# Optimization experiments

Measured on AMD Instinct MI355X. Metric: run time of the kernel, lower is better.

Reference implementation:

```python
import jax, jax.numpy as jnp
import numpy as np
from jax import lax

D, H, HD, DEPTH = 200, 10, 20, 12   # embed_dim, heads, head_dim, depth
NCH, A = 64, 8                       # EEG channels x time windows -> 512 patches (+cls)
NUM_REL = (2 * NCH - 1) * (2 * A - 1) + 3  # 1908


def make_rel_index(wh, ww):
    # exact port of the torch relative_position_index construction
    coords = np.stack(np.meshgrid(np.arange(wh), np.arange(ww), indexing='ij')).reshape(2, -1)
    rel = (coords[:, :, None] - coords[:, None, :]).transpose(1, 2, 0)
    rel[..., 0] += wh - 1
    rel[..., 1] += ww - 1
    rel[..., 0] *= 2 * ww - 1
    n = wh * ww + 1
    num_rel = (2 * wh - 1) * (2 * ww - 1) + 3
    idx = np.zeros((n, n), dtype=np.int32)
    idx[1:, 1:] = rel.sum(-1)
    idx[0, :] = num_rel - 3
    idx[:, 0] = num_rel - 2
    idx[0, 0] = num_rel - 1
    return idx


def gelu(x):
    return jax.nn.gelu(x, approximate=False)


def layer_norm(x, g, b, eps=1e-6):
    m = x.mean(-1, keepdims=True)
    v = ((x - m) ** 2).mean(-1, keepdims=True)
    return (x - m) * lax.rsqrt(v + eps) * g + b


def group_norm(x, g, b, groups=4, eps=1e-5):
    B, C, Hh, W = x.shape
    xr = x.reshape(B, groups, C // groups, Hh, W)
    m = xr.mean((2, 3, 4), keepdims=True)
    v = ((xr - m) ** 2).mean((2, 3, 4), keepdims=True)
    xr = ((xr - m) * lax.rsqrt(v + eps)).reshape(B, C, Hh, W)
    return xr * g[None, :, None, None] + b[None, :, None, None]


def conv2d(x, w, b, stride, pad):
    y = lax.conv_general_dilated(x, w, window_strides=stride, padding=pad,
                                 dimension_numbers=('NCHW', 'OIHW', 'NCHW'))
    return y + b[None, :, None, None]


def setup_inputs() -> dict:
    B = 8
    key = jax.random.key(0)
    ks = iter(jax.random.split(key, 40))
    rn = lambda shape, s=0.02: jax.random.normal(next(ks), shape, dtype=jnp.float32) * s
    z = lambda shape: jnp.zeros(shape, jnp.float32)
    o = lambda shape: jnp.ones(shape, jnp.float32)
    inp = {}
    inp['x'] = jax.random.normal(next(ks), (B, NCH, A, 200), dtype=jnp.float32)
    inp['conv1_w'] = rn((8, 1, 1, 15), 0.1); inp['conv1_b'] = z(8)
    inp['gn1_g'] = o(8); inp['gn1_b'] = z(8)
    inp['conv2_w'] = rn((8, 8, 1, 3), 0.1); inp['conv2_b'] = z(8)
    inp['gn2_g'] = o(8); inp['gn2_b'] = z(8)
    inp['conv3_w'] = rn((8, 8, 1, 3), 0.1); inp['conv3_b'] = z(8)
    inp['gn3_g'] = o(8); inp['gn3_b'] = z(8)
    inp['cls_token'] = rn((1, 1, D)); inp['pos_embed'] = rn((1, NCH + 1, D))
    inp['time_embed'] = rn((1, 16, D))
    inp['ln1_g'] = o((DEPTH, D)); inp['ln1_b'] = z((DEPTH, D))
    inp['qkv_w'] = rn((DEPTH, 3 * D, D))
    inp['rel_bias_table'] = rn((DEPTH, NUM_REL, H))
    inp['proj_w'] = rn((DEPTH, D, D)); inp['proj_b'] = z((DEPTH, D))
    inp['gamma1'] = 0.1 * o((DEPTH, D))
    inp['ln2_g'] = o((DEPTH, D)); inp['ln2_b'] = z((DEPTH, D))
    inp['fc1_w'] = rn((DEPTH, 4 * D, D)); inp['fc1_b'] = z((DEPTH, 4 * D))
    inp['fc2_w'] = rn((DEPTH, D, 4 * D)); inp['fc2_b'] = z((DEPTH, D))
    inp['gamma2'] = 0.1 * o((DEPTH, D))
    inp['fc_norm_g'] = o(D); inp['fc_norm_b'] = z(D)
    inp['head_w'] = rn((4, D)); inp['head_b'] = z(4)
    inp['rel_pos_index'] = jnp.asarray(make_rel_index(NCH, A))
    return inp


def reference(x, conv1_w, conv1_b, gn1_g, gn1_b, conv2_w, conv2_b, gn2_g, gn2_b,
              conv3_w, conv3_b, gn3_g, gn3_b, cls_token, pos_embed, time_embed,
              ln1_g, ln1_b, qkv_w, rel_bias_table, proj_w, proj_b, gamma1,
              ln2_g, ln2_b, fc1_w, fc1_b, fc2_w, fc2_b, gamma2,
              fc_norm_g, fc_norm_b, head_w, head_b, rel_pos_index):
    B = x.shape[0]
    # TemporalConv patch embed: (B, NCH, A, 200) -> (B, NCH*A, D)
    h = x.reshape(B, 1, NCH * A, -1)
    h = gelu(group_norm(conv2d(h, conv1_w, conv1_b, (1, 8), [(0, 0), (7, 7)]), gn1_g, gn1_b))
    h = gelu(group_norm(conv2d(h, conv2_w, conv2_b, (1, 1), [(0, 0), (1, 1)]), gn2_g, gn2_b))
    h = gelu(group_norm(conv2d(h, conv3_w, conv3_b, (1, 1), [(0, 0), (1, 1)]), gn3_g, gn3_b))
    h = h.transpose(0, 2, 3, 1).reshape(B, NCH * A, D)  # 'B C NA T -> B NA (T C)'
    # cls token + per-electrode pos embed + temporal embed
    h = jnp.concatenate([jnp.broadcast_to(cls_token, (B, 1, D)), h], axis=1)
    pos_p = jnp.repeat(pos_embed[:, 1:, None, :], A, axis=2).reshape(1, NCH * A, D)
    h = h + jnp.concatenate([pos_embed[:, :1], pos_p], axis=1)
    te = jnp.broadcast_to(time_embed[:, None, :A, :], (1, NCH, A, D)).reshape(1, NCH * A, D)
    h = jnp.concatenate([h[:, :1], h[:, 1:] + te], axis=1)
    N = h.shape[1]  # 513
    scale = HD ** -0.5
    for d in range(DEPTH):
        y = layer_norm(h, ln1_g[d], ln1_b[d])
        qkv = (y @ qkv_w[d].T).reshape(B, N, 3, H, HD).transpose(2, 0, 3, 1, 4)
        q, k, v = qkv[0], qkv[1], qkv[2]
        attn = jnp.einsum('bhnd,bhmd->bhnm', q * scale, k)
        attn = attn + rel_bias_table[d][rel_pos_index].transpose(2, 0, 1)[None]
        attn = jax.nn.softmax(attn, axis=-1)
        o = jnp.einsum('bhnm,bhmd->bhnd', attn, v)
        o = o.transpose(0, 2, 1, 3).reshape(B, N, D) @ proj_w[d].T + proj_b[d]
        h = h + gamma1[d] * o
        y = layer_norm(h, ln2_g[d], ln2_b[d])
        y = gelu(y @ fc1_w[d].T + fc1_b[d]) @ fc2_w[d].T + fc2_b[d]
        h = h + gamma2[d] * y
    pooled = layer_norm(h[:, 1:].mean(1), fc_norm_g, fc_norm_b)  # use_mean_pooling
    return pooled @ head_w.T + head_b
```

## Files before the change

### kernel.cpp

```cpp
#include <hip/hip_runtime.h>
#include <math.h>

#define DEV static __device__ __forceinline__

typedef __attribute__((ext_vector_type(8))) short bf16x8;
typedef __attribute__((ext_vector_type(4))) float f32x4;

DEV float gelu_exact(float x) {
    return 0.5f * x * (1.0f + erff(x * 0.70710678118654752f));
}

DEV short f2bf(float f) {
    union { float f; unsigned u; } v; v.f = f;
    unsigned r = v.u + 0x7FFF + ((v.u >> 16) & 1);
    return (short)(r >> 16);
}

DEV float bf2f(unsigned short b) {
    union { unsigned u; float f; } v; v.u = ((unsigned)b) << 16;
    return v.f;
}

DEV unsigned pack2bf(float a, float b) {
    return ((unsigned)(unsigned short)f2bf(a)) | (((unsigned)(unsigned short)f2bf(b)) << 16);
}

DEV void gload_lds16(const void* g, void* lds) {
    __builtin_amdgcn_global_load_lds(
        (const __attribute__((address_space(1))) void*)g,
        (__attribute__((address_space(3))) void*)lds, 16, 0, 0);
}

__global__ void conv1_kernel(const float* __restrict__ x, const float* __restrict__ w,
                             const float* __restrict__ bias, float* __restrict__ out) {
    int idx = blockIdx.x * blockDim.x + threadIdx.x;
    const int total = 8 * 8 * 512 * 25;
    if (idx >= total) return;
    int ow = idx % 25;
    int p  = (idx / 25) % 512;
    int oc = (idx / (25 * 512)) % 8;
    int b  = idx / (25 * 512 * 8);
    const float* xp = x + b * 512 * 200 + p * 200;
    const float* wp = w + oc * 15;
    float acc = bias[oc];
    int t0 = ow * 8 - 7;
#pragma unroll
    for (int k = 0; k < 15; k++) {
        int t = t0 + k;
        if (t >= 0 && t < 200) acc += wp[k] * xp[t];
    }
    out[idx] = acc;
}

__global__ void conv3x1_kernel(const float* __restrict__ in, const float* __restrict__ w,
                               const float* __restrict__ bias, float* __restrict__ out) {
    int idx = blockIdx.x * blockDim.x + threadIdx.x;
    const int total = 8 * 8 * 512 * 25;
    if (idx >= total) return;
    int ow = idx % 25;
    int p  = (idx / 25) % 512;
    int oc = (idx / 12800) & 7;
    int b  = idx / 102400;
    float acc = bias[oc];
#pragma unroll
    for (int ic = 0; ic < 8; ic++) {
        const float* ip = in + b * 102400 + ic * 12800 + p * 25;
        const float* wp = w + oc * 24 + ic * 3;
        if (ow > 0)  acc += wp[0] * ip[ow - 1];
        acc += wp[1] * ip[ow];
        if (ow < 24) acc += wp[2] * ip[ow + 1];
    }
    out[idx] = acc;
}

__global__ void gn_stats_kernel(const float* __restrict__ buf, float* __restrict__ stats) {
    int b = blockIdx.x >> 2, g = blockIdx.x & 3;
    const float* base = buf + b * 102400 + g * 2 * 12800;
    float s = 0.f, s2 = 0.f;
    for (int l = threadIdx.x; l < 25600; l += 256) {
        float v = base[l];
        s += v; s2 += v * v;
    }
    __shared__ float ss[256], ss2[256];
    ss[threadIdx.x] = s; ss2[threadIdx.x] = s2;
    __syncthreads();
    for (int o = 128; o; o >>= 1) {
        if (threadIdx.x < o) { ss[threadIdx.x] += ss[threadIdx.x + o]; ss2[threadIdx.x] += ss2[threadIdx.x + o]; }
        __syncthreads();
    }
    if (threadIdx.x == 0) {
        float m = ss[0] / 25600.f;
        float v = ss2[0] / 25600.f - m * m;
        stats[blockIdx.x * 2] = m;
        stats[blockIdx.x * 2 + 1] = v;
    }
}

__global__ void gn_apply_kernel(float* __restrict__ buf, const float* __restrict__ stats,
                                const float* __restrict__ g, const float* __restrict__ bb) {
    int idx = blockIdx.x * blockDim.x + threadIdx.x;
    if (idx >= 8 * 102400) return;
    int c = (idx / 12800) & 7;
    int b = idx / 102400;
    int grp = c >> 1;
    float m = stats[(b * 4 + grp) * 2];
    float v = stats[(b * 4 + grp) * 2 + 1];
    float val = (buf[idx] - m) * rsqrtf(v + 1e-5f) * g[c] + bb[c];
    buf[idx] = gelu_exact(val);
}

__global__ void embed_kernel(const float* __restrict__ conv, const float* __restrict__ cls,
                             const float* __restrict__ pos, const float* __restrict__ te,
                             float* __restrict__ h) {
    int idx = blockIdx.x * blockDim.x + threadIdx.x;
    if (idx >= 8 * 513 * 200) return;
    int d = idx % 200;
    int n = (idx / 200) % 513;
    int b = idx / (200 * 513);
    float val;
    if (n == 0) {
        val = cls[d] + pos[d];
    } else {
        int p = n - 1;
        int t = d >> 3;
        int c = d & 7;
        val = conv[b * 102400 + c * 12800 + p * 25 + t];
        int ch = p >> 3, tw = p & 7;
        val += pos[(1 + ch) * 200 + d] + te[tw * 200 + d];
    }
    h[idx] = val;
}

__global__ void convpad_kernel(const float* __restrict__ src, short* __restrict__ dst,
                               int R, int K, int KP) {
    int idx = blockIdx.x * blockDim.x + threadIdx.x;
    if (idx >= R * KP) return;
    int r = idx / KP, c = idx % KP;
    dst[idx] = (c < K) ? f2bf(src[r * K + c]) : (short)0;
}

__global__ __launch_bounds__(256) void bias_lds_kernel(const float* __restrict__ table,
                                                       const int* __restrict__ ridx,
                                                       short* __restrict__ bias) {
    __shared__ float tl[1908];
    const int qt = blockIdx.x, hh = blockIdx.y, d = blockIdx.z;
    const float* tab = table + d * 19080;
    for (int i = threadIdx.x; i < 1908; i += 256) tl[i] = tab[i * 10 + hh];
    __syncthreads();
    const int q0 = qt * 64;
    const int nrows = min(64, 513 - q0);
    short* obase = bias + ((size_t)d * 10 + hh) * 513 * 576;
    for (int lin = threadIdx.x; lin < nrows * 144; lin += 256) {
        int r = lin / 144, j = lin % 144;
        int q = q0 + r;
        const int* rp = ridx + q * 513;
        int k0 = j * 4;
        float v[4];
#pragma unroll
        for (int e = 0; e < 4; e++) {
            int k = k0 + e;
            v[e] = (k < 513) ? tl[rp[k]] : 0.f;
        }
        uint2 pk;
        pk.x = pack2bf(v[0], v[1]);
        pk.y = pack2bf(v[2], v[3]);
        *(uint2*)&obase[(size_t)q * 576 + k0] = pk;
    }
}

__global__ __launch_bounds__(256) void ln_kernel(const float* __restrict__ in,
                                                 const float* __restrict__ g,
                                                 const float* __restrict__ b,
                                                 short* __restrict__ out) {
    int row = blockIdx.x * 4 + (threadIdx.x >> 6);
    int lane = threadIdx.x & 63;
    const float* x = in + (size_t)row * 200;
    float v[4];
    float s = 0.f;
#pragma unroll
    for (int i = 0; i < 4; i++) {
        int d = lane + i * 64;
        v[i] = (d < 200) ? x[d] : 0.f;
        s += v[i];
    }
#pragma unroll
    for (int o = 32; o; o >>= 1) s += __shfl_xor(s, o);
    float mean = s * (1.f / 200.f);
    float s2 = 0.f;
#pragma unroll
    for (int i = 0; i < 4; i++) {
        int d = lane + i * 64;
        float dv = (d < 200) ? (v[i] - mean) : 0.f;
        s2 += dv * dv;
    }
#pragma unroll
    for (int o = 32; o; o >>= 1) s2 += __shfl_xor(s2, o);
    float rstd = rsqrtf(s2 * (1.f / 200.f) + 1e-6f);
#pragma unroll
    for (int i = 0; i < 4; i++) {
        int d = lane + i * 64;
        float val = (d < 200) ? (v[i] - mean) * rstd * g[d] + b[d] : 0.f;
        out[(size_t)row * 256 + d] = f2bf(val);
    }
}

template <int EPI, int BM, int BN>
__global__ __launch_bounds__(256) void gemm_bf(const short* __restrict__ A,
                                               const short* __restrict__ W,
                                               float* __restrict__ Cf,
                                               short* __restrict__ Cb,
                                               const float* __restrict__ res,
                                               const float* __restrict__ bias,
                                               const float* __restrict__ gamma,
                                               int M, int N, int KP, int ldc, int NPout,
                                               short* __restrict__ Qb = nullptr,
                                               short* __restrict__ Kb = nullptr,
                                               short* __restrict__ Vt = nullptr) {
    constexpr int WM = BM / 2, WN = BN / 2;
    constexpr int AM = WM / 16, BNr = WN / 16;
    constexpr int LOADS = (BM + BN) / 32;
    __shared__ __align__(16) short Ss[2][(BM + BN) * 64];

    const int tid = threadIdx.x;
    const int w = tid >> 6, l = tid & 63;
    const int wm = (w >> 1) * WM, wn = (w & 1) * WN;
    const int bm = blockIdx.y * BM, bn = blockIdx.x * BN;

    f32x4 acc[AM][BNr] = {};

    auto stage = [&](int buf, int k0) {
#pragma unroll
        for (int it = 0; it < LOADS; it++) {
            int lin = it * 256 + tid;
            int row = lin >> 3, slot = lin & 7;
            int srcslot = slot ^ (row & 7);
            const short* g;
            if (it * 32 < BM) {
                g = A + (size_t)(bm + row) * KP + k0 + srcslot * 8;
            } else {
                g = W + (size_t)(bn + row - BM) * KP + k0 + srcslot * 8;
            }
            gload_lds16(g, (char*)Ss[buf] + lin * 16);
        }
    };

    const int nk = KP >> 6;
    stage(0, 0);
    int cur = 0;
    for (int kstep = 0; kstep < nk; kstep++) {
        if (kstep + 1 < nk) {
            stage(cur ^ 1, (kstep + 1) << 6);
            if constexpr (LOADS == 6) asm volatile("s_waitcnt vmcnt(6)" ::: "memory");
            else                      asm volatile("s_waitcnt vmcnt(4)" ::: "memory");
        } else {
            asm volatile("s_waitcnt vmcnt(0)" ::: "memory");
        }
        __builtin_amdgcn_s_barrier();

        const char* Sc = (const char*)Ss[cur];
#pragma unroll
        for (int kk = 0; kk < 2; kk++) {
            const int kbyte = kk * 64 + (l >> 4) * 16;
            bf16x8 af[AM], bfr[BNr];
#pragma unroll
            for (int i = 0; i < AM; i++) {
                int r = wm + i * 16 + (l & 15);
                af[i] = *(const bf16x8*)(Sc + r * 128 + (kbyte ^ ((r & 7) << 4)));
            }
#pragma unroll
            for (int j = 0; j < BNr; j++) {
                int r = BM + wn + j * 16 + (l & 15);
                bfr[j] = *(const bf16x8*)(Sc + r * 128 + (kbyte ^ ((r & 7) << 4)));
            }
#pragma unroll
            for (int i = 0; i < AM; i++)
#pragma unroll
                for (int j = 0; j < BNr; j++)
                    acc[i][j] = __builtin_amdgcn_mfma_f32_16x16x32_bf16(af[i], bfr[j], acc[i][j], 0, 0, 0);
        }
        __builtin_amdgcn_s_barrier();
        cur ^= 1;
    }

    const int col0 = bn + wn + (l & 15);
    const int rbase = (l >> 4) * 4;
#pragma unroll
    for (int i = 0; i < AM; i++) {
#pragma unroll
        for (int r = 0; r < 4; r++) {
            int gm = bm + wm + i * 16 + rbase + r;
            if (gm >= M) continue;
#pragma unroll
            for (int j = 0; j < BNr; j++) {
                int gn = col0 + j * 16;
                float v = acc[i][j][r];
                if (EPI == 0) {
                    if (gn < N) Cf[(size_t)gm * ldc + gn] = v;
                } else if (EPI == 1) {
                    if (gn < N) Cf[(size_t)gm * ldc + gn] =
                        res[(size_t)gm * ldc + gn] + gamma[gn] * (v + bias[gn]);
                } else if (EPI == 2) {
                    if (gn < NPout)
                        Cb[(size_t)gm * ldc + gn] = (gn < N) ? f2bf(gelu_exact(v + bias[gn])) : (short)0;
                } else {
                    if (gn < 600) {
                        int bb2 = gm / 513, n = gm - bb2 * 513;
                        if (gn < 200) {
                            int hq = gn / 20, dq = gn - hq * 20;
                            Qb[((size_t)(bb2 * 10 + hq) * 576 + n) * 32 + dq] =
                                f2bf(v * 0.22360679774997896f);
                        } else if (gn < 400) {
                            int gk = gn - 200, hk = gk / 20, dk = gk - hk * 20;
                            Kb[((size_t)(bb2 * 10 + hk) * 576 + n) * 32 + dk] = f2bf(v);
                        } else {
                            int gv = gn - 400, hv = gv / 20, dv2 = gv - hv * 20;
                            Vt[((size_t)(bb2 * 10 + hv) * 32 + dv2) * 576 + n] = f2bf(v);
                        }
                    }
                }
            }
        }
    }
}

__global__ __launch_bounds__(256) void attn_mfma2(const short* __restrict__ Qb,
                                                  const short* __restrict__ Kb,
                                                  const short* __restrict__ Vt,
                                                  const short* __restrict__ biasb,
                                                  short* __restrict__ ob) {
    __shared__ __align__(16) short Klds[2][64 * 32];
    __shared__ __align__(16) short Vlds[2][32 * 64];
    __shared__ __align__(16) short Blds[2][64 * 64];
    __shared__ __align__(16) short Pl[4 * 16 * 72];

    const int orig = blockIdx.x;
    const int wg = (orig & 7) * 90 + (orig >> 3);
    const int hh = wg / 72;
    const int rem = wg % 72;
    const int qt = rem >> 3, b = rem & 7;

    const int t = threadIdx.x, wave = t >> 6, l = t & 63;
    const int lq = l & 15, hi = l >> 4;
    const int n = qt * 64 + wave * 16 + lq;
    const int nc = min(n, 512);

    const size_t bh = (size_t)(b * 10 + hh);
    const short* Kbase = Kb + bh * 576 * 32;
    const short* Vbase = Vt + bh * 32 * 576;
    const short* Bbase = biasb + (size_t)hh * 513 * 576;

    bf16x8 qf = *(const bf16x8*)&Qb[(bh * 576 + nc) * 32 + hi * 8];

    const int krow = t >> 2, kch = t & 3;
    const short* ksrc = Kbase + (size_t)krow * 32 + (kch ^ ((krow >> 2) & 3)) * 8;
    const int vrow = t >> 3, vch = t & 7;
    const short* vsrc = Vbase + (size_t)vrow * 576 + (vch ^ (vrow & 7)) * 8;
    const int b0row = t >> 3, b0ch = t & 7;
    const short* bsrc0 = Bbase + (size_t)min(qt * 64 + b0row, 512) * 576 + (b0ch ^ (b0row & 7)) * 8;
    const int b1row = 32 + (t >> 3);
    const short* bsrc1 = Bbase + (size_t)min(qt * 64 + b1row, 512) * 576 + (b0ch ^ (b1row & 7)) * 8;

    float mrun = -1e30f, lsum = 0.f;
    f32x4 oacc0 = {}, oacc1 = {};
    const f32x4 zero4 = {};

    gload_lds16(ksrc, (char*)Klds[0] + t * 16);
    gload_lds16(vsrc, (char*)Vlds[0] + t * 16);
    gload_lds16(bsrc0, (char*)Blds[0] + t * 16);
    gload_lds16(bsrc1, (char*)Blds[0] + 4096 + t * 16);

    int cur = 0;
    for (int kt = 0; kt < 9; kt++) {
        const int koff = kt * 64;
        if (kt < 8) {
            const int knext = koff + 64;
            gload_lds16(ksrc + (size_t)knext * 32, (char*)Klds[cur ^ 1] + t * 16);
            gload_lds16(vsrc + knext, (char*)Vlds[cur ^ 1] + t * 16);
            gload_lds16(bsrc0 + knext, (char*)Blds[cur ^ 1] + t * 16);
            gload_lds16(bsrc1 + knext, (char*)Blds[cur ^ 1] + 4096 + t * 16);
            asm volatile("s_waitcnt vmcnt(4)" ::: "memory");
        } else {
            asm volatile("s_waitcnt vmcnt(0)" ::: "memory");
        }
        __builtin_amdgcn_s_barrier();

        const short* Kc = Klds[cur];
        const short* Vc = Vlds[cur];
        const short* Bc = Blds[cur];

        f32x4 s[4];
#pragma unroll
        for (int c = 0; c < 4; c++) {
            int r = c * 16 + lq;
            bf16x8 kf = *(const bf16x8*)((const char*)Kc + r * 64 + ((hi ^ ((lq >> 2) & 3)) << 4));
            s[c] = __builtin_amdgcn_mfma_f32_16x16x32_bf16(kf, qf, zero4, 0, 0, 0);
        }

        const int brow = wave * 16 + lq;
        float sv[4][4];
        float tm = -1e30f;
#pragma unroll
        for (int c = 0; c < 4; c++) {
            uint2 bl = *(const uint2*)((const char*)Bc + brow * 128 +
                                       (((2 * c + (hi >> 1)) ^ (lq & 7)) << 4) + (hi & 1) * 8);
            float bv[4] = { bf2f((unsigned short)(bl.x & 0xFFFF)), bf2f((unsigned short)(bl.x >> 16)),
                            bf2f((unsigned short)(bl.y & 0xFFFF)), bf2f((unsigned short)(bl.y >> 16)) };
            int kglob = koff + c * 16 + hi * 4;
#pragma unroll
            for (int r = 0; r < 4; r++) {
                float val = s[c][r] + bv[r];
                if (kglob + r > 512) val = -1e30f;
                sv[c][r] = val;
                tm = fmaxf(tm, val);
            }
        }
        tm = fmaxf(tm, __shfl_xor(tm, 16));
        tm = fmaxf(tm, __shfl_xor(tm, 32));
        float mnew = fmaxf(mrun, tm);
        float resc = __expf(mrun - mnew);
        mrun = mnew;

        float ts = 0.f;
#pragma unroll
        for (int c = 0; c < 4; c++) {
            float p0 = __expf(sv[c][0] - mnew);
            float p1 = __expf(sv[c][1] - mnew);
            float p2 = __expf(sv[c][2] - mnew);
            float p3 = __expf(sv[c][3] - mnew);
            ts += (p0 + p1) + (p2 + p3);
            uint2 pk;
            pk.x = pack2bf(p0, p1);
            pk.y = pack2bf(p2, p3);
            *(uint2*)&Pl[wave * 1152 + lq * 72 + c * 16 + hi * 4] = pk;
        }
        ts += __shfl_xor(ts, 16);
        ts += __shfl_xor(ts, 32);
        lsum = lsum * resc + ts;
        oacc0 *= resc;
        oacc1 *= resc;

#pragma unroll
        for (int kc = 0; kc < 2; kc++) {
            bf16x8 pf = *(const bf16x8*)&Pl[wave * 1152 + lq * 72 + kc * 32 + hi * 8];
            bf16x8 vf0 = *(const bf16x8*)((const char*)Vc + lq * 128 +
                                          (((kc * 4 + hi) ^ (lq & 7)) << 4));
            bf16x8 vf1 = *(const bf16x8*)((const char*)Vc + (16 + lq) * 128 +
                                          (((kc * 4 + hi) ^ (lq & 7)) << 4));
            oacc0 = __builtin_amdgcn_mfma_f32_16x16x32_bf16(vf0, pf, oacc0, 0, 0, 0);
            oacc1 = __builtin_amdgcn_mfma_f32_16x16x32_bf16(vf1, pf, oacc1, 0, 0, 0);
        }

        __builtin_amdgcn_s_barrier();
        cur ^= 1;
    }

    if (n < 513) {
        float inv = 1.f / lsum;
        short* op = ob + (size_t)(b * 513 + n) * 256 + hh * 20;
        {
            uint2 pk;
            pk.x = pack2bf(oacc0[0] * inv, oacc0[1] * inv);
            pk.y = pack2bf(oacc0[2] * inv, oacc0[3] * inv);
            *(uint2*)&op[hi * 4] = pk;
        }
        if (hi == 0) {
            uint2 pk;
            pk.x = pack2bf(oacc1[0] * inv, oacc1[1] * inv);
            pk.y = pack2bf(oacc1[2] * inv, oacc1[3] * inv);
            *(uint2*)&op[16] = pk;
        }
    }
}

__global__ __launch_bounds__(256) void final_kernel(const float* __restrict__ h,
                                                    const float* __restrict__ g,
                                                    const float* __restrict__ bb,
                                                    const float* __restrict__ hw,
                                                    const float* __restrict__ hb,
                                                    float* __restrict__ out) {
    __shared__ float pool[256];
    __shared__ float red[256];
    int b = blockIdx.x, t = threadIdx.x;
    float s = 0.f;
    if (t < 200) {
        const float* hp = h + b * 513 * 200 + 200 + t;
        for (int p = 0; p < 512; p++) s += hp[p * 200];
        s *= (1.f / 512.f);
    }
    pool[t] = (t < 200) ? s : 0.f;
    red[t] = pool[t];
    __syncthreads();
    for (int o = 128; o; o >>= 1) {
        if (t < o) red[t] += red[t + o];
        __syncthreads();
    }
    float mean = red[0] / 200.f;
    __syncthreads();
    float dv = (t < 200) ? (pool[t] - mean) : 0.f;
    red[t] = dv * dv;
    __syncthreads();
    for (int o = 128; o; o >>= 1) {
        if (t < o) red[t] += red[t + o];
        __syncthreads();
    }
    float var = red[0] / 200.f;
    float rstd = rsqrtf(var + 1e-6f);
    __syncthreads();
    if (t < 200) pool[t] = (pool[t] - mean) * rstd * g[t] + bb[t];
    __syncthreads();
    if (t < 4) {
        float acc = hb[t];
        for (int d2 = 0; d2 < 200; d2++) acc += pool[d2] * hw[t * 200 + d2];
        out[b * 4 + t] = acc;
    }
}

extern "C" void kernel_launch(void* const* d_in, const int* in_sizes, int n_in,
                              void* d_out, int out_size, void* d_ws, size_t ws_size,
                              hipStream_t stream) {
    const float* x        = (const float*)d_in[0];
    const float* conv1_w  = (const float*)d_in[1];
    const float* conv1_b  = (const float*)d_in[2];
    const float* gn1_g    = (const float*)d_in[3];
    const float* gn1_b    = (const float*)d_in[4];
    const float* conv2_w  = (const float*)d_in[5];
    const float* conv2_b  = (const float*)d_in[6];
    const float* gn2_g    = (const float*)d_in[7];
    const float* gn2_b    = (const float*)d_in[8];
    const float* conv3_w  = (const float*)d_in[9];
    const float* conv3_b  = (const float*)d_in[10];
    const float* gn3_g    = (const float*)d_in[11];
    const float* gn3_b    = (const float*)d_in[12];
    const float* cls_tok  = (const float*)d_in[13];
    const float* pos_emb  = (const float*)d_in[14];
    const float* time_emb = (const float*)d_in[15];
    const float* ln1_g    = (const float*)d_in[16];
    const float* ln1_b    = (const float*)d_in[17];
    const float* qkv_w    = (const float*)d_in[18];
    const float* rel_tab  = (const float*)d_in[19];
    const float* proj_w   = (const float*)d_in[20];
    const float* proj_b   = (const float*)d_in[21];
    const float* gamma1   = (const float*)d_in[22];
    const float* ln2_g    = (const float*)d_in[23];
    const float* ln2_b    = (const float*)d_in[24];
    const float* fc1_w    = (const float*)d_in[25];
    const float* fc1_b    = (const float*)d_in[26];
    const float* fc2_w    = (const float*)d_in[27];
    const float* fc2_b    = (const float*)d_in[28];
    const float* gamma2   = (const float*)d_in[29];
    const float* fcn_g    = (const float*)d_in[30];
    const float* fcn_b    = (const float*)d_in[31];
    const float* head_w   = (const float*)d_in[32];
    const float* head_b   = (const float*)d_in[33];
    const int*   rel_idx  = (const int*)d_in[34];

    char* p = (char*)d_ws;
    float* h    = (float*)p; p += 3283200;
    char* qreg = p;
    float* c1   = (float*)qreg;
    float* c2   = c1 + 819200;
    short* Qb   = (short*)qreg;
    short* Kb   = Qb + 1474560;
    short* Vt   = Kb + 1474560;
    short* mlp  = (short*)qreg;
    p += 9849600;
    short* y    = (short*)p; p += 2101248;
    short* ob   = (short*)p; p += 2101248;
    short* wqkv = (short*)p; p += 3686400;
    short* wproj= (short*)p; p += 1228800;
    short* wfc1 = (short*)p; p += 4915200;
    short* wfc2 = (short*)p; p += 3993600;
    short* biasb= (short*)p; p += 12 * 5909760;
    float* stats= (float*)p;

    convpad_kernel<<<(7200 * 256 + 255) / 256, 256, 0, stream>>>(qkv_w, wqkv, 7200, 200, 256);
    convpad_kernel<<<(2400 * 256 + 255) / 256, 256, 0, stream>>>(proj_w, wproj, 2400, 200, 256);
    convpad_kernel<<<(9600 * 256 + 255) / 256, 256, 0, stream>>>(fc1_w, wfc1, 9600, 200, 256);
    convpad_kernel<<<(2400 * 832 + 255) / 256, 256, 0, stream>>>(fc2_w, wfc2, 2400, 800, 832);
    bias_lds_kernel<<<dim3(9, 10, 12), 256, 0, stream>>>(rel_tab, rel_idx, biasb);
    hipMemsetAsync(ob, 0, 2101248, stream);

    conv1_kernel<<<3200, 256, 0, stream>>>(x, conv1_w, conv1_b, c1);
    gn_stats_kernel<<<32, 256, 0, stream>>>(c1, stats);
    gn_apply_kernel<<<3200, 256, 0, stream>>>(c1, stats, gn1_g, gn1_b);
    conv3x1_kernel<<<3200, 256, 0, stream>>>(c1, conv2_w, conv2_b, c2);
    gn_stats_kernel<<<32, 256, 0, stream>>>(c2, stats);
    gn_apply_kernel<<<3200, 256, 0, stream>>>(c2, stats, gn2_g, gn2_b);
    conv3x1_kernel<<<3200, 256, 0, stream>>>(c2, conv3_w, conv3_b, c1);
    gn_stats_kernel<<<32, 256, 0, stream>>>(c1, stats);
    gn_apply_kernel<<<3200, 256, 0, stream>>>(c1, stats, gn3_g, gn3_b);
    embed_kernel<<<(820800 + 255) / 256, 256, 0, stream>>>(c1, cls_tok, pos_emb, time_emb, h);

    hipMemsetAsync(Qb, 0, 3 * 1474560 * 2, stream);

    for (int d = 0; d < 12; d++) {
        ln_kernel<<<1026, 256, 0, stream>>>(h, ln1_g + d * 200, ln1_b + d * 200, y);
        gemm_bf<3, 64, 128><<<dim3(5, 65), 256, 0, stream>>>(y, wqkv + d * 153600,
                                                             nullptr, nullptr, nullptr, nullptr, nullptr,
                                                             4104, 600, 256, 0, 0, Qb, Kb, Vt);
        attn_mfma2<<<720, 256, 0, stream>>>(Qb, Kb, Vt, biasb + (size_t)d * 2954880, ob);
        gemm_bf<1, 64, 64><<<dim3(4, 65), 256, 0, stream>>>(ob, wproj + d * 51200, h, nullptr,
                                                            h, proj_b + d * 200, gamma1 + d * 200,
                                                            4104, 200, 256, 200, 0);
        ln_kernel<<<1026, 256, 0, stream>>>(h, ln2_g + d * 200, ln2_b + d * 200, y);
        gemm_bf<2, 64, 128><<<dim3(7, 65), 256, 0, stream>>>(y, wfc1 + d * 204800, nullptr, mlp,
                                                             nullptr, fc1_b + d * 800, nullptr,
                                                             4104, 800, 256, 832, 832);
        gemm_bf<1, 64, 64><<<dim3(4, 65), 256, 0, stream>>>(mlp, wfc2 + d * 166400, h, nullptr,
                                                            h, fc2_b + d * 200, gamma2 + d * 200,
                                                            4104, 200, 832, 200, 0);
    }

    final_kernel<<<8, 256, 0, stream>>>(h, fcn_g, fcn_b, head_w, head_b, (float*)d_out);
}
```

Baseline: 1.095 ms.

## Fuse LayerNorm into QKV and FC1 GEMM prologues; widen bias-table stores

Removes the standalone LayerNorm kernels. The QKV and FC1 GEMMs now read the fp32 residual stream directly, normalise each 64-row tile in registers and write swizzled bf16 rows into LDS as the A operand. Only the weight tiles are double-buffered from global memory. This drops the 24 LN launches per forward and the round trip through the bf16 y buffer, but each column-block recomputes LayerNorm for its rows and variance now uses the one-pass E[x^2]-mean^2 form. The bias expansion kernel also writes 8 bf16 values per store instead of 4.

```diff
diff --git a/kernel.cpp b/kernel.cpp
--- a/kernel.cpp
+++ b/kernel.cpp
@@ -150,132 +150,118 @@
     const int q0 = qt * 64;
     const int nrows = min(64, 513 - q0);
     short* obase = bias + ((size_t)d * 10 + hh) * 513 * 576;
-    for (int lin = threadIdx.x; lin < nrows * 144; lin += 256) {
-        int r = lin / 144, j = lin % 144;
+    for (int lin = threadIdx.x; lin < nrows * 72; lin += 256) {
+        int r = lin / 72, j = lin % 72;
         int q = q0 + r;
         const int* rp = ridx + q * 513;
-        int k0 = j * 4;
-        float v[4];
-#pragma unroll
-        for (int e = 0; e < 4; e++) {
+        int k0 = j * 8;
+        float v[8];
+#pragma unroll
+        for (int e = 0; e < 8; e++) {
             int k = k0 + e;
             v[e] = (k < 513) ? tl[rp[k]] : 0.f;
         }
-        uint2 pk;
+        uint4 pk;
         pk.x = pack2bf(v[0], v[1]);
         pk.y = pack2bf(v[2], v[3]);
-        *(uint2*)&obase[(size_t)q * 576 + k0] = pk;
-    }
-}
-
-__global__ __launch_bounds__(256) void ln_kernel(const float* __restrict__ in,
-                                                 const float* __restrict__ g,
-                                                 const float* __restrict__ b,
-                                                 short* __restrict__ out) {
-    int row = blockIdx.x * 4 + (threadIdx.x >> 6);
-    int lane = threadIdx.x & 63;
-    const float* x = in + (size_t)row * 200;
-    float v[4];
-    float s = 0.f;
-#pragma unroll
-    for (int i = 0; i < 4; i++) {
-        int d = lane + i * 64;
-        v[i] = (d < 200) ? x[d] : 0.f;
-        s += v[i];
-    }
-#pragma unroll
-    for (int o = 32; o; o >>= 1) s += __shfl_xor(s, o);
-    float mean = s * (1.f / 200.f);
-    float s2 = 0.f;
-#pragma unroll
-    for (int i = 0; i < 4; i++) {
-        int d = lane + i * 64;
-        float dv = (d < 200) ? (v[i] - mean) : 0.f;
-        s2 += dv * dv;
-    }
-#pragma unroll
-    for (int o = 32; o; o >>= 1) s2 += __shfl_xor(s2, o);
-    float rstd = rsqrtf(s2 * (1.f / 200.f) + 1e-6f);
-#pragma unroll
-    for (int i = 0; i < 4; i++) {
-        int d = lane + i * 64;
-        float val = (d < 200) ? (v[i] - mean) * rstd * g[d] + b[d] : 0.f;
-        out[(size_t)row * 256 + d] = f2bf(val);
-    }
-}
-
-template <int EPI, int BM, int BN>
-__global__ __launch_bounds__(256) void gemm_bf(const short* __restrict__ A,
-                                               const short* __restrict__ W,
-                                               float* __restrict__ Cf,
-                                               short* __restrict__ Cb,
-                                               const float* __restrict__ res,
-                                               const float* __restrict__ bias,
-                                               const float* __restrict__ gamma,
-                                               int M, int N, int KP, int ldc, int NPout,
-                                               short* __restrict__ Qb = nullptr,
-                                               short* __restrict__ Kb = nullptr,
-                                               short* __restrict__ Vt = nullptr) {
-    constexpr int WM = BM / 2, WN = BN / 2;
-    constexpr int AM = WM / 16, BNr = WN / 16;
-    constexpr int LOADS = (BM + BN) / 32;
-    __shared__ __align__(16) short Ss[2][(BM + BN) * 64];
+        pk.z = pack2bf(v[4], v[5]);
+        pk.w = pack2bf(v[6], v[7]);
+        *(uint4*)&obase[(size_t)q * 576 + k0] = pk;
+    }
+}
+
+template <int EPI>
+__global__ __launch_bounds__(256) void lngemm_bf(const float* __restrict__ H,
+                                                 const short* __restrict__ W,
+                                                 const float* __restrict__ lng,
+                                                 const float* __restrict__ lnb,
+                                                 short* __restrict__ Cb,
+                                                 const float* __restrict__ bias,
+                                                 int M, int N, int ldc, int NPout,
+                                                 short* __restrict__ Qb = nullptr,
+                                                 short* __restrict__ Kb = nullptr,
+                                                 short* __restrict__ Vt = nullptr) {
+    __shared__ __align__(16) short At[64 * 256];
+    __shared__ __align__(16) short Ws[2][128 * 64];
 
     const int tid = threadIdx.x;
     const int w = tid >> 6, l = tid & 63;
-    const int wm = (w >> 1) * WM, wn = (w & 1) * WN;
-    const int bm = blockIdx.y * BM, bn = blockIdx.x * BN;
-
-    f32x4 acc[AM][BNr] = {};
-
-    auto stage = [&](int buf, int k0) {
-#pragma unroll
-        for (int it = 0; it < LOADS; it++) {
+    const int wm = (w >> 1) * 32, wn = (w & 1) * 64;
+    const int bm = blockIdx.y * 64, bn = blockIdx.x * 128;
+
+    auto stageW = [&](int buf, int k0) {
+#pragma unroll
+        for (int it = 0; it < 4; it++) {
             int lin = it * 256 + tid;
             int row = lin >> 3, slot = lin & 7;
             int srcslot = slot ^ (row & 7);
-            const short* g;
-            if (it * 32 < BM) {
-                g = A + (size_t)(bm + row) * KP + k0 + srcslot * 8;
-            } else {
-                g = W + (size_t)(bn + row - BM) * KP + k0 + srcslot * 8;
-            }
-            gload_lds16(g, (char*)Ss[buf] + lin * 16);
+            gload_lds16(W + (size_t)(bn + row) * 256 + k0 + srcslot * 8,
+                        (char*)Ws[buf] + lin * 16);
         }
     };
 
-    const int nk = KP >> 6;
-    stage(0, 0);
+    stageW(0, 0);
+
+    float4 gv = {0, 0, 0, 0}, bv = {0, 0, 0, 0};
+    if (l < 50) {
+        gv = *(const float4*)&lng[l * 4];
+        bv = *(const float4*)&lnb[l * 4];
+    }
+    for (int rr = 0; rr < 16; rr++) {
+        int row = w * 16 + rr;
+        int gm = bm + row;
+        float4 hv = {0, 0, 0, 0};
+        if (gm < M && l < 50) hv = *(const float4*)&H[(size_t)gm * 200 + l * 4];
+        float s = hv.x + hv.y + hv.z + hv.w;
+        float q = hv.x * hv.x + hv.y * hv.y + hv.z * hv.z + hv.w * hv.w;
+#pragma unroll
+        for (int o = 32; o; o >>= 1) { s += __shfl_xor(s, o); q += __shfl_xor(q, o); }
+        float mean = s * (1.f / 200.f);
+        float var = q * (1.f / 200.f) - mean * mean;
+        float rstd = rsqrtf(var + 1e-6f);
+        float v0 = (l < 50) ? (hv.x - mean) * rstd * gv.x + bv.x : 0.f;
+        float v1 = (l < 50) ? (hv.y - mean) * rstd * gv.y + bv.y : 0.f;
+        float v2 = (l < 50) ? (hv.z - mean) * rstd * gv.z + bv.z : 0.f;
+        float v3 = (l < 50) ? (hv.w - mean) * rstd * gv.w + bv.w : 0.f;
+        uint2 pk;
+        pk.x = pack2bf(v0, v1);
+        pk.y = pack2bf(v2, v3);
+        *(uint2*)((char*)At + row * 512 + ((((l >> 1) ^ (row & 7)) << 4) | ((l & 1) * 8))) = pk;
+    }
+    asm volatile("s_waitcnt lgkmcnt(0)" ::: "memory");
+
+    f32x4 acc[2][4] = {};
     int cur = 0;
-    for (int kstep = 0; kstep < nk; kstep++) {
-        if (kstep + 1 < nk) {
-            stage(cur ^ 1, (kstep + 1) << 6);
-            if constexpr (LOADS == 6) asm volatile("s_waitcnt vmcnt(6)" ::: "memory");
-            else                      asm volatile("s_waitcnt vmcnt(4)" ::: "memory");
+#pragma unroll
+    for (int kstep = 0; kstep < 4; kstep++) {
+        if (kstep < 3) {
+            stageW(cur ^ 1, (kstep + 1) * 64);
+            asm volatile("s_waitcnt vmcnt(4)" ::: "memory");
         } else {
             asm volatile("s_waitcnt vmcnt(0)" ::: "memory");
         }
         __builtin_amdgcn_s_barrier();
 
-        const char* Sc = (const char*)Ss[cur];
+        const char* Wc = (const char*)Ws[cur];
 #pragma unroll
         for (int kk = 0; kk < 2; kk++) {
-            const int kbyte = kk * 64 + (l >> 4) * 16;
-            bf16x8 af[AM], bfr[BNr];
-#pragma unroll
-            for (int i = 0; i < AM; i++) {
+            const int kbyteW = kk * 64 + (l >> 4) * 16;
+            const int g = kstep * 8 + kk * 4 + (l >> 4);
+            bf16x8 af[2], bfr[4];
+#pragma unroll
+            for (int i = 0; i < 2; i++) {
                 int r = wm + i * 16 + (l & 15);
-                af[i] = *(const bf16x8*)(Sc + r * 128 + (kbyte ^ ((r & 7) << 4)));
-            }
-#pragma unroll
-            for (int j = 0; j < BNr; j++) {
-                int r = BM + wn + j * 16 + (l & 15);
-                bfr[j] = *(const bf16x8*)(Sc + r * 128 + (kbyte ^ ((r & 7) << 4)));
-            }
-#pragma unroll
-            for (int i = 0; i < AM; i++)
-#pragma unroll
-                for (int j = 0; j < BNr; j++)
+                af[i] = *(const bf16x8*)((const char*)At + r * 512 + ((g ^ (r & 7)) << 4));
+            }
+#pragma unroll
+            for (int j = 0; j < 4; j++) {
+                int r = wn + j * 16 + (l & 15);
+                bfr[j] = *(const bf16x8*)(Wc + r * 128 + (kbyteW ^ ((r & 7) << 4)));
+            }
+#pragma unroll
+            for (int i = 0; i < 2; i++)
+#pragma unroll
+                for (int j = 0; j < 4; j++)
                     acc[i][j] = __builtin_amdgcn_mfma_f32_16x16x32_bf16(af[i], bfr[j], acc[i][j], 0, 0, 0);
         }
         __builtin_amdgcn_s_barrier();
@@ -285,21 +271,16 @@
     const int col0 = bn + wn + (l & 15);
     const int rbase = (l >> 4) * 4;
 #pragma unroll
-    for (int i = 0; i < AM; i++) {
+    for (int i = 0; i < 2; i++) {
 #pragma unroll
         for (int r = 0; r < 4; r++) {
             int gm = bm + wm + i * 16 + rbase + r;
             if (gm >= M) continue;
 #pragma unroll
-            for (int j = 0; j < BNr; j++) {
+            for (int j = 0; j < 4; j++) {
                 int gn = col0 + j * 16;
                 float v = acc[i][j][r];
-                if (EPI == 0) {
-                    if (gn < N) Cf[(size_t)gm * ldc + gn] = v;
-                } else if (EPI == 1) {
-                    if (gn < N) Cf[(size_t)gm * ldc + gn] =
-                        res[(size_t)gm * ldc + gn] + gamma[gn] * (v + bias[gn]);
-                } else if (EPI == 2) {
+                if (EPI == 2) {
                     if (gn < NPout)
                         Cb[(size_t)gm * ldc + gn] = (gn < N) ? f2bf(gelu_exact(v + bias[gn])) : (short)0;
                 } else {
@@ -313,11 +294,104 @@
                             int gk = gn - 200, hk = gk / 20, dk = gk - hk * 20;
                             Kb[((size_t)(bb2 * 10 + hk) * 576 + n) * 32 + dk] = f2bf(v);
                         } else {
-                            int gv = gn - 400, hv = gv / 20, dv2 = gv - hv * 20;
-                            Vt[((size_t)(bb2 * 10 + hv) * 32 + dv2) * 576 + n] = f2bf(v);
+                            int gv2 = gn - 400, hv2 = gv2 / 20, dv2 = gv2 - hv2 * 20;
+                            Vt[((size_t)(bb2 * 10 + hv2) * 32 + dv2) * 576 + n] = f2bf(v);
                         }
                     }
                 }
+            }
+        }
+    }
+}
+
+template <int EPI, int BM, int BN>
+__global__ __launch_bounds__(256) void gemm_bf(const short* __restrict__ A,
+                                               const short* __restrict__ W,
+                                               float* __restrict__ Cf,
+                                               const float* __restrict__ res,
+                                               const float* __restrict__ bias,
+                                               const float* __restrict__ gamma,
+                                               int M, int N, int KP, int ldc) {
+    constexpr int WM = BM / 2, WN = BN / 2;
+    constexpr int AM = WM / 16, BNr = WN / 16;
+    constexpr int LOADS = (BM + BN) / 32;
+    __shared__ __align__(16) short Ss[2][(BM + BN) * 64];
+
+    const int tid = threadIdx.x;
+    const int w = tid >> 6, l = tid & 63;
+    const int wm = (w >> 1) * WM, wn = (w & 1) * WN;
+    const int bm = blockIdx.y * BM, bn = blockIdx.x * BN;
+
+    f32x4 acc[AM][BNr] = {};
+
+    auto stage = [&](int buf, int k0) {
+#pragma unroll
+        for (int it = 0; it < LOADS; it++) {
+            int lin = it * 256 + tid;
+            int row = lin >> 3, slot = lin & 7;
+            int srcslot = slot ^ (row & 7);
+            const short* g;
+            if (it * 32 < BM) {
+                g = A + (size_t)(bm + row) * KP + k0 + srcslot * 8;
+            } else {
+                g = W + (size_t)(bn + row - BM) * KP + k0 + srcslot * 8;
+            }
+            gload_lds16(g, (char*)Ss[buf] + lin * 16);
+        }
+    };
+
+    const int nk = KP >> 6;
+    stage(0, 0);
+    int cur = 0;
+    for (int kstep = 0; kstep < nk; kstep++) {
+        if (kstep + 1 < nk) {
+            stage(cur ^ 1, (kstep + 1) << 6);
+            if constexpr (LOADS == 6) asm volatile("s_waitcnt vmcnt(6)" ::: "memory");
+            else                      asm volatile("s_waitcnt vmcnt(4)" ::: "memory");
+        } else {
+            asm volatile("s_waitcnt vmcnt(0)" ::: "memory");
+        }
+        __builtin_amdgcn_s_barrier();
+
+        const char* Sc = (const char*)Ss[cur];
+#pragma unroll
+        for (int kk = 0; kk < 2; kk++) {
+            const int kbyte = kk * 64 + (l >> 4) * 16;
+            bf16x8 af[AM], bfr[BNr];
+#pragma unroll
+            for (int i = 0; i < AM; i++) {
+                int r = wm + i * 16 + (l & 15);
+                af[i] = *(const bf16x8*)(Sc + r * 128 + (kbyte ^ ((r & 7) << 4)));
+            }
+#pragma unroll
+            for (int j = 0; j < BNr; j++) {
+                int r = BM + wn + j * 16 + (l & 15);
+                bfr[j] = *(const bf16x8*)(Sc + r * 128 + (kbyte ^ ((r & 7) << 4)));
+            }
+#pragma unroll
+            for (int i = 0; i < AM; i++)
+#pragma unroll
+                for (int j = 0; j < BNr; j++)
+                    acc[i][j] = __builtin_amdgcn_mfma_f32_16x16x32_bf16(af[i], bfr[j], acc[i][j], 0, 0, 0);
+        }
+        __builtin_amdgcn_s_barrier();
+        cur ^= 1;
+    }
+
+    const int col0 = bn + wn + (l & 15);
+    const int rbase = (l >> 4) * 4;
+#pragma unroll
+    for (int i = 0; i < AM; i++) {
+#pragma unroll
+        for (int r = 0; r < 4; r++) {
+            int gm = bm + wm + i * 16 + rbase + r;
+            if (gm >= M) continue;
+#pragma unroll
+            for (int j = 0; j < BNr; j++) {
+                int gn = col0 + j * 16;
+                if (gn < N)
+                    Cf[(size_t)gm * ldc + gn] =
+                        res[(size_t)gm * ldc + gn] + gamma[gn] * (acc[i][j][r] + bias[gn]);
             }
         }
     }
@@ -564,7 +638,6 @@
     short* Vt   = Kb + 1474560;
     short* mlp  = (short*)qreg;
     p += 9849600;
-    short* y    = (short*)p; p += 2101248;
     short* ob   = (short*)p; p += 2101248;
     short* wqkv = (short*)p; p += 3686400;
     short* wproj= (short*)p; p += 1228800;
@@ -594,21 +667,21 @@
     hipMemsetAsync(Qb, 0, 3 * 1474560 * 2, stream);
 
     for (int d = 0; d < 12; d++) {
-        ln_kernel<<<1026, 256, 0, stream>>>(h, ln1_g + d * 200, ln1_b + d * 200, y);
-        gemm_bf<3, 64, 128><<<dim3(5, 65), 256, 0, stream>>>(y, wqkv + d * 153600,
-                                                             nullptr, nullptr, nullptr, nullptr, nullptr,
-                                                             4104, 600, 256, 0, 0, Qb, Kb, Vt);
+        lngemm_bf<3><<<dim3(5, 65), 256, 0, stream>>>(h, wqkv + d * 153600,
+                                                      ln1_g + d * 200, ln1_b + d * 200,
+                                                      nullptr, nullptr,
+                                                      4104, 600, 0, 0, Qb, Kb, Vt);
         attn_mfma2<<<720, 256, 0, stream>>>(Qb, Kb, Vt, biasb + (size_t)d * 2954880, ob);
-        gemm_bf<1, 64, 64><<<dim3(4, 65), 256, 0, stream>>>(ob, wproj + d * 51200, h, nullptr,
+        gemm_bf<1, 64, 64><<<dim3(4, 65), 256, 0, stream>>>(ob, wproj + d * 51200, h,
                                                             h, proj_b + d * 200, gamma1 + d * 200,
-                                                            4104, 200, 256, 200, 0);
-        ln_kernel<<<1026, 256, 0, stream>>>(h, ln2_g + d * 200, ln2_b + d * 200, y);
-        gemm_bf<2, 64, 128><<<dim3(7, 65), 256, 0, stream>>>(y, wfc1 + d * 204800, nullptr, mlp,
-                                                             nullptr, fc1_b + d * 800, nullptr,
-                                                             4104, 800, 256, 832, 832);
-        gemm_bf<1, 64, 64><<<dim3(4, 65), 256, 0, stream>>>(mlp, wfc2 + d * 166400, h, nullptr,
+                                                            4104, 200, 256, 200);
+        lngemm_bf<2><<<dim3(7, 65), 256, 0, stream>>>(h, wfc1 + d * 204800,
+                                                      ln2_g + d * 200, ln2_b + d * 200,
+                                                      mlp, fc1_b + d * 800,
+                                                      4104, 800, 832, 832);
+        gemm_bf<1, 64, 64><<<dim3(4, 65), 256, 0, stream>>>(mlp, wfc2 + d * 166400, h,
                                                             h, fc2_b + d * 200, gamma2 + d * 200,
-                                                            4104, 200, 832, 200, 0);
+                                                            4104, 200, 832, 200);
     }
 
     final_kernel<<<8, 256, 0, stream>>>(h, fcn_g, fcn_b, head_w, head_b, (float*)d_out);
```

Measured after the change: 1.305 ms. 19.2% more time.
